# Kernel tuning notes

Measured on AMD Instinct MI355X. Metric: run time of the kernel, lower is better.

The kernel has to match this reference:

```python
import jax, jax.numpy as jnp
import numpy as np

NFEAT, NHID, NHEADS = 512, 64, 8
ALPHA = 0.2
NEG = -9e15  # torch uses -9000000000000000.0


def _xavier(key, shape, gain=1.414):
    fan_in, fan_out = shape[-2], shape[-1]
    bound = gain * np.sqrt(6.0 / (fan_in + fan_out))
    return jax.random.uniform(key, shape, jnp.float32, -bound, bound)


def setup_inputs() -> dict:
    key = jax.random.key(0)
    ks = jax.random.split(key, 6)
    N = 2048
    x = jax.random.normal(ks[0], (N, NFEAT), jnp.float32)
    adj = jax.random.randint(ks[1], (N, N), 0, 2, jnp.int32)
    # per-head stacked params for the two attention banks
    W1 = _xavier(ks[2], (NHEADS, NFEAT, NHID))
    a1 = _xavier(ks[3], (NHEADS, 2 * NHID, 1))
    W2 = _xavier(ks[4], (NHEADS, NFEAT, NHID))
    a2 = _xavier(ks[5], (NHEADS, 2 * NHID, 1))
    return {"x": x, "adj": adj, "W1": W1, "a1": a1, "W2": W2, "a2": a2}


def _gat_bank(x, adj_mask, W, a):
    """All heads of one GraphAttentionLayer bank, vectorized over heads.
    x: [N, F], W: [H, F, O], a: [H, 2O, 1]. Returns concat output [N, H*O]
    and attention [H, N, N]."""
    N = x.shape[0]
    Wh = jnp.einsum('nf,hfo->hno', x, W)               # [H, N, O]
    a_src = a[:, :NHID, 0]                             # [H, O]
    a_dst = a[:, NHID:, 0]                             # [H, O]
    Wh1 = jnp.einsum('hno,ho->hn', Wh, a_src)          # [H, N]
    Wh2 = jnp.einsum('hno,ho->hn', Wh, a_dst)          # [H, N]
    e = Wh1[:, :, None] + Wh2[:, None, :]              # [H, N, N]
    e = jnp.where(e > 0, e, ALPHA * e)                 # LeakyReLU
    e = jnp.where(adj_mask[None, :, :], e, NEG)
    attention = jax.nn.softmax(e, axis=-1)             # [H, N, N]
    h_prime = jnp.einsum('hnm,hmo->hno', attention, Wh)
    out = jax.nn.elu(h_prime)                          # concat=True -> elu
    # torch.cat over heads along feature dim: [N, H*O]
    out = jnp.transpose(out, (1, 0, 2)).reshape(N, NHEADS * NHID)
    return out, attention


def reference(x, adj, W1, a1, W2, a2):
    adj_mask = adj > 0
    # dropout layers are no-ops in eval mode
    h1, att1 = _gat_bank(x, adj_mask, W1, a1)
    h1 = jax.nn.elu(h1)
    h2, att2 = _gat_bank(h1, adj_mask, W2, a2)
    h2 = jax.nn.elu(h2)
    return h2, att1, att2
```

## Files before the change

kernel.cpp:

```cpp
#include <hip/hip_runtime.h>
#include <hip/hip_bf16.h>


typedef __attribute__((ext_vector_type(8))) short bf16x8;
typedef __attribute__((ext_vector_type(4))) float f32x4;

__device__ __forceinline__ float bf2f(unsigned short u) {
    return __uint_as_float(((unsigned int)u) << 16);
}
__device__ __forceinline__ unsigned short f2bf(float f) {
    __hip_bfloat16 h = __float2bfloat16(f);
    return __builtin_bit_cast(unsigned short, h);
}
__device__ __forceinline__ float elu1(float x) { return x > 0.f ? x : expm1f(x); }

__global__ __launch_bounds__(256) void adjbits_kernel(
    const int* __restrict__ adj, unsigned long long* __restrict__ gbits) {
    int g = blockIdx.x * 256 + threadIdx.x;
    unsigned long long m = __ballot(adj[g] > 0);
    if ((threadIdx.x & 63) == 0) gbits[g >> 6] = m;
}

__global__ __launch_bounds__(256) void reorder_w_kernel(
    const float* __restrict__ W, unsigned short* __restrict__ WpHi,
    unsigned short* __restrict__ WpLo) {
    int i = blockIdx.x * 256 + threadIdx.x;
    int o = i & 63;
    int k = (i >> 6) & 511;
    int h = i >> 15;
    float v = W[i];
    unsigned short hi = f2bf(v);
    unsigned short lo = f2bf(v - bf2f(hi));
    long idx = (((h * 16) + (k >> 5)) * 64 + o) * 32 + (k & 31);
    WpHi[idx] = hi;
    WpLo[idx] = lo;
}

__global__ __launch_bounds__(256, 2) void gemm1_kernel(
    const float* __restrict__ A,
    const unsigned short* __restrict__ BpHi, const unsigned short* __restrict__ BpLo,
    const float* __restrict__ avec,
    unsigned short* __restrict__ Whp, float* __restrict__ s1, float* __restrict__ s2) {
    __shared__ float accred[2][64][20];
    const int bx   = blockIdx.x;
    const int h    = bx >> 6;
    const int mt   = bx & 63;
    const int tid  = threadIdx.x;
    const int wave = tid >> 6;
    const int lane = tid & 63;
    const int quad = lane >> 4;
    const int m16  = lane & 15;
    const int rw   = wave & 1;
    const int kw   = wave >> 1;
    const int rowbase = mt * 32 + rw * 16;

    const float* Arow = A + (long)(rowbase + m16) * 512 + kw * 256 + quad * 8;
    const long boff = ((long)(h * 16 + kw * 8) * 64 + m16) * 32 + quad * 8;
    const unsigned short* BH = BpHi + boff;
    const unsigned short* BL = BpLo + boff;

    f32x4 acc[4];
#pragma unroll
    for (int t = 0; t < 4; ++t)
#pragma unroll
        for (int r = 0; r < 4; ++r) acc[t][r] = 0.f;

    for (int kb = 0; kb < 8; ++kb) {
        const float* ap = Arow + kb * 32;
        bf16x8 ahi, alo;
#pragma unroll
        for (int j = 0; j < 8; ++j) {
            float v = ap[j];
            unsigned short hv = f2bf(v);
            ahi[j] = (short)hv;
            alo[j] = (short)f2bf(v - bf2f(hv));
        }
        const unsigned short* bh0 = BH + (long)kb * 2048;
        const unsigned short* bl0 = BL + (long)kb * 2048;
#pragma unroll
        for (int t = 0; t < 4; ++t) {
            bf16x8 bh = *reinterpret_cast<const bf16x8*>(bh0 + t * 512);
            bf16x8 bl = *reinterpret_cast<const bf16x8*>(bl0 + t * 512);
            acc[t] = __builtin_amdgcn_mfma_f32_16x16x32_bf16(alo, bh, acc[t], 0, 0, 0);
            acc[t] = __builtin_amdgcn_mfma_f32_16x16x32_bf16(ahi, bl, acc[t], 0, 0, 0);
            acc[t] = __builtin_amdgcn_mfma_f32_16x16x32_bf16(ahi, bh, acc[t], 0, 0, 0);
        }
    }

    if (kw == 1) {
#pragma unroll
        for (int t = 0; t < 4; ++t)
            *reinterpret_cast<f32x4*>(&accred[rw][t * 16 + m16][quad * 4]) = acc[t];
    }
    __syncthreads();
    if (kw == 1) return;

#pragma unroll
    for (int t = 0; t < 4; ++t) {
        f32x4 o = *reinterpret_cast<const f32x4*>(&accred[rw][t * 16 + m16][quad * 4]);
#pragma unroll
        for (int r = 0; r < 4; ++r) acc[t][r] += o[r];
    }

    float aS[4], aD[4];
#pragma unroll
    for (int t = 0; t < 4; ++t) {
        aS[t] = avec[(h << 7) + t * 16 + m16];
        aD[t] = avec[(h << 7) + 64 + t * 16 + m16];
    }
#pragma unroll
    for (int r = 0; r < 4; ++r) {
        float t1 = 0.f, t2 = 0.f;
#pragma unroll
        for (int t = 0; t < 4; ++t) {
            float v = acc[t][r];
            t1 = fmaf(v, aS[t], t1);
            t2 = fmaf(v, aD[t], t2);
        }
#pragma unroll
        for (int off = 1; off < 16; off <<= 1) {
            t1 += __shfl_xor(t1, off);
            t2 += __shfl_xor(t2, off);
        }
        if (m16 == 0) {
            int row = rowbase + quad * 4 + r;
            s1[(h << 11) + row] = t1;
            s2[(h << 11) + row] = t2;
        }
    }

#pragma unroll
    for (int t = 0; t < 4; ++t) {
        const int col = t * 16 + m16;
#pragma unroll
        for (int r = 0; r < 4; ++r) {
            const int row = rowbase + quad * 4 + r;
            long idx = (((long)(h * 64 + (row >> 5)) * 64 + col) << 5) + (row & 31);
            Whp[idx] = f2bf(acc[t][r]);
        }
    }
}

__global__ __launch_bounds__(256, 4) void fused_att_kernel(
    const float* __restrict__ s1g, const float* __restrict__ s2g,
    const unsigned int* __restrict__ gbits,
    const unsigned short* __restrict__ Whp,
    float* __restrict__ att, float* __restrict__ hout) {
    __shared__ unsigned int lbits[16 * 65];
    __shared__ float ls2[2048];
    __shared__ float lmax[4][16];
    __shared__ float lsum[4][16];
    __shared__ float accred[3][64][20];
    __shared__ f32x4 pstage[4][16][9];

    const int bx   = blockIdx.x;
    const int h    = bx >> 7;
    const int row0 = (bx & 127) << 4;
    const int tid  = threadIdx.x;
    const int wq   = tid >> 6;
    const int lane = tid & 63;
    const int quad = lane >> 4;
    const int m16  = lane & 15;

#pragma unroll
    for (int i = 0; i < 4; ++i) {
        int idx = i * 256 + tid;
        lbits[(idx >> 6) * 65 + (idx & 63)] = gbits[((row0 + (idx >> 6)) << 6) + (idx & 63)];
    }
    const float4* s2v4 = reinterpret_cast<const float4*>(s2g + (h << 11));
#pragma unroll
    for (int i = 0; i < 2; ++i) {
        int idx = i * 256 + tid;
        reinterpret_cast<float4*>(ls2)[idx] = s2v4[idx];
    }
    __syncthreads();

    const float s1i = s1g[(h << 11) + row0 + m16];

    float mx = -INFINITY;
    for (int i = 0; i < 16; ++i) {
        const int jt = wq * 16 + i;
        unsigned int word = lbits[m16 * 65 + jt];
        float4 sa = *reinterpret_cast<const float4*>(ls2 + jt * 32 + quad * 8);
        float4 sb = *reinterpret_cast<const float4*>(ls2 + jt * 32 + quad * 8 + 4);
        float sv[8] = {sa.x, sa.y, sa.z, sa.w, sb.x, sb.y, sb.z, sb.w};
#pragma unroll
        for (int u = 0; u < 8; ++u)
            mx = fmaxf(mx, ((word >> (quad * 8 + u)) & 1u) ? sv[u] : -INFINITY);
    }
    mx = fmaxf(mx, __shfl_xor(mx, 16));
    mx = fmaxf(mx, __shfl_xor(mx, 32));
    if (lane < 16) lmax[wq][m16] = mx;
    __syncthreads();
    const float Ms2 = fmaxf(fmaxf(lmax[0][m16], lmax[1][m16]),
                            fmaxf(lmax[2][m16], lmax[3][m16]));
    const float ebar = s1i + Ms2;
    const float m = fmaxf(ebar, 0.2f * ebar);
    const bool am = (m == -INFINITY);

    float lp = 0.f;
    for (int i = 0; i < 16; ++i) {
        const int jt = wq * 16 + i;
        unsigned int word = lbits[m16 * 65 + jt];
        float4 sa = *reinterpret_cast<const float4*>(ls2 + jt * 32 + quad * 8);
        float4 sb = *reinterpret_cast<const float4*>(ls2 + jt * 32 + quad * 8 + 4);
        float sv[8] = {sa.x, sa.y, sa.z, sa.w, sb.x, sb.y, sb.z, sb.w};
#pragma unroll
        for (int u = 0; u < 8; ++u) {
            float e = s1i + sv[u];
            e = fmaxf(e, 0.2f * e);
            lp += ((word >> (quad * 8 + u)) & 1u) ? __expf(e - m) : 0.f;
        }
    }
    lp += __shfl_xor(lp, 16);
    lp += __shfl_xor(lp, 32);
    if (lane < 16) lsum[wq][m16] = lp;
    __syncthreads();
    const float l = lsum[0][m16] + lsum[1][m16] + lsum[2][m16] + lsum[3][m16];
    const float invl = am ? 0.f : 1.f / l;
    const float fallb = 1.f / 2048.f;

    f32x4 acc[4];
#pragma unroll
    for (int t = 0; t < 4; ++t)
#pragma unroll
        for (int r = 0; r < 4; ++r) acc[t][r] = 0.f;

    const unsigned short* BW = Whp + ((long)(h << 12) + m16) * 32 + quad * 8;
    float* attbase = att + (long)h * 4194304 + (long)row0 * 2048;
    const int fr = lane >> 3;
    const int fc = lane & 7;

    for (int i = 0; i < 16; ++i) {
        const int jt = wq * 16 + i;
        unsigned int word = lbits[m16 * 65 + jt];
        float4 sa = *reinterpret_cast<const float4*>(ls2 + jt * 32 + quad * 8);
        float4 sb = *reinterpret_cast<const float4*>(ls2 + jt * 32 + quad * 8 + 4);
        float sv[8] = {sa.x, sa.y, sa.z, sa.w, sb.x, sb.y, sb.z, sb.w};
        float p[8];
        bf16x8 af;
#pragma unroll
        for (int u = 0; u < 8; ++u) {
            float e = s1i + sv[u];
            e = fmaxf(e, 0.2f * e);
            float pv = ((word >> (quad * 8 + u)) & 1u) ? __expf(e - m) * invl : 0.f;
            p[u] = am ? fallb : pv;
            af[u] = (short)f2bf(p[u]);
        }
        f32x4 plo, phi;
        plo[0] = p[0]; plo[1] = p[1]; plo[2] = p[2]; plo[3] = p[3];
        phi[0] = p[4]; phi[1] = p[5]; phi[2] = p[6]; phi[3] = p[7];
        pstage[wq][m16][quad * 2]     = plo;
        pstage[wq][m16][quad * 2 + 1] = phi;

        const unsigned short* b0 = BW + (long)jt * 2048;
#pragma unroll
        for (int t = 0; t < 4; ++t) {
            bf16x8 bf = *reinterpret_cast<const bf16x8*>(b0 + t * 512);
            acc[t] = __builtin_amdgcn_mfma_f32_16x16x32_bf16(af, bf, acc[t], 0, 0, 0);
        }

#pragma unroll
        for (int half = 0; half < 2; ++half) {
            const int r = half * 8 + fr;
            f32x4 v = pstage[wq][r][fc];
            __builtin_nontemporal_store(
                v, reinterpret_cast<f32x4*>(attbase + (long)r * 2048 + jt * 32 + fc * 4));
        }
    }

    if (wq > 0) {
#pragma unroll
        for (int t = 0; t < 4; ++t)
            *reinterpret_cast<f32x4*>(&accred[wq - 1][t * 16 + m16][quad * 4]) = acc[t];
    }
    __syncthreads();
    if (wq == 0) {
#pragma unroll
        for (int t = 0; t < 4; ++t) {
            const int col = t * 16 + m16;
#pragma unroll
            for (int w = 0; w < 3; ++w) {
                f32x4 o = *reinterpret_cast<const f32x4*>(&accred[w][col][quad * 4]);
#pragma unroll
                for (int r = 0; r < 4; ++r) acc[t][r] += o[r];
            }
#pragma unroll
            for (int r = 0; r < 4; ++r) {
                const int row = row0 + quad * 4 + r;
                hout[(row << 9) + (h << 6) + col] = elu1(elu1(acc[t][r]));
            }
        }
    }
}

extern "C" void kernel_launch(void* const* d_in, const int* in_sizes, int n_in,
                              void* d_out, int out_size, void* d_ws, size_t ws_size,
                              hipStream_t stream) {
    const float* x  = (const float*)d_in[0];
    const int* adj  = (const int*)d_in[1];
    const float* W1 = (const float*)d_in[2];
    const float* a1 = (const float*)d_in[3];
    const float* W2 = (const float*)d_in[4];
    const float* a2 = (const float*)d_in[5];

    float* out  = (float*)d_out;
    float* att1 = out + 1048576;
    float* att2 = att1 + 33554432;

    char* w = (char*)d_ws;
    unsigned short* WpHi  = (unsigned short*)(w);
    unsigned short* WpLo  = (unsigned short*)(w + 524288);
    unsigned short* Whp   = (unsigned short*)(w + 1048576);
    float* s1             = (float*)(w + 3145728);
    float* s2             = (float*)(w + 3211264);
    unsigned long long* gbits = (unsigned long long*)(w + 3276800);
    float* x2             = (float*)(w + 3801088);

    const unsigned int* gbits32 = (const unsigned int*)gbits;

    adjbits_kernel<<<16384, 256, 0, stream>>>(adj, gbits);

    reorder_w_kernel<<<1024, 256, 0, stream>>>(W1, WpHi, WpLo);
    gemm1_kernel<<<512, 256, 0, stream>>>(x, WpHi, WpLo, a1, Whp, s1, s2);
    fused_att_kernel<<<1024, 256, 0, stream>>>(s1, s2, gbits32, Whp, att1, x2);

    reorder_w_kernel<<<1024, 256, 0, stream>>>(W2, WpHi, WpLo);
    gemm1_kernel<<<512, 256, 0, stream>>>(x2, WpHi, WpLo, a2, Whp, s1, s2);
    fused_att_kernel<<<1024, 256, 0, stream>>>(s1, s2, gbits32, Whp, att2, out);
}
```

Measured before the change: 358.6 us.

## Use global per-head s2 max as softmax shift and cache unnormalized exps

Computes a per-head global maximum of s2 in the GEMM epilogue via atomicMax on order-preserving keys, and uses it as the softmax shift. This removes the per-row masked max pass and one block barrier. The unnormalized exponentials are cached in registers as bf16 and fed directly to the MFMA, with normalization applied once to the output accumulators. This drops the second exp pass. The risks are more register pressure from the 16-entry cached array and possible underflow when the global max is far above a row's masked max. Written attention values are also now rounded through bf16 before scaling.

```diff
diff --git a/kernel.cpp b/kernel.cpp
--- a/kernel.cpp
+++ b/kernel.cpp
@@ -13,6 +13,14 @@
     return __builtin_bit_cast(unsigned short, h);
 }
 __device__ __forceinline__ float elu1(float x) { return x > 0.f ? x : expm1f(x); }
+
+__device__ __forceinline__ unsigned fkey(float f) {
+    unsigned b = __float_as_uint(f);
+    return (b & 0x80000000u) ? ~b : (b | 0x80000000u);
+}
+__device__ __forceinline__ float funkey(unsigned k) {
+    return __uint_as_float((k & 0x80000000u) ? (k ^ 0x80000000u) : ~k);
+}
 
 __global__ __launch_bounds__(256) void adjbits_kernel(
     const int* __restrict__ adj, unsigned long long* __restrict__ gbits) {
@@ -23,7 +31,8 @@
 
 __global__ __launch_bounds__(256) void reorder_w_kernel(
     const float* __restrict__ W, unsigned short* __restrict__ WpHi,
-    unsigned short* __restrict__ WpLo) {
+    unsigned short* __restrict__ WpLo, unsigned* __restrict__ Mmax) {
+    if (blockIdx.x == 0 && threadIdx.x < 8) Mmax[threadIdx.x] = 0u;
     int i = blockIdx.x * 256 + threadIdx.x;
     int o = i & 63;
     int k = (i >> 6) & 511;
@@ -40,7 +49,8 @@
     const float* __restrict__ A,
     const unsigned short* __restrict__ BpHi, const unsigned short* __restrict__ BpLo,
     const float* __restrict__ avec,
-    unsigned short* __restrict__ Whp, float* __restrict__ s1, float* __restrict__ s2) {
+    unsigned short* __restrict__ Whp, float* __restrict__ s1, float* __restrict__ s2,
+    unsigned* __restrict__ Mmax) {
     __shared__ float accred[2][64][20];
     const int bx   = blockIdx.x;
     const int h    = bx >> 6;
@@ -108,6 +118,7 @@
         aS[t] = avec[(h << 7) + t * 16 + m16];
         aD[t] = avec[(h << 7) + 64 + t * 16 + m16];
     }
+    float s2max = -INFINITY;
 #pragma unroll
     for (int r = 0; r < 4; ++r) {
         float t1 = 0.f, t2 = 0.f;
@@ -122,12 +133,16 @@
             t1 += __shfl_xor(t1, off);
             t2 += __shfl_xor(t2, off);
         }
+        s2max = fmaxf(s2max, t2);
         if (m16 == 0) {
             int row = rowbase + quad * 4 + r;
             s1[(h << 11) + row] = t1;
             s2[(h << 11) + row] = t2;
         }
     }
+    s2max = fmaxf(s2max, __shfl_xor(s2max, 16));
+    s2max = fmaxf(s2max, __shfl_xor(s2max, 32));
+    if (lane == 0) atomicMax(Mmax + h, fkey(s2max));
 
 #pragma unroll
     for (int t = 0; t < 4; ++t) {
@@ -145,11 +160,12 @@
     const float* __restrict__ s1g, const float* __restrict__ s2g,
     const unsigned int* __restrict__ gbits,
     const unsigned short* __restrict__ Whp,
+    const unsigned* __restrict__ Mmax,
     float* __restrict__ att, float* __restrict__ hout) {
     __shared__ unsigned int lbits[16 * 65];
     __shared__ float ls2[2048];
-    __shared__ float lmax[4][16];
     __shared__ float lsum[4][16];
+    __shared__ float linv[16];
     __shared__ float accred[3][64][20];
     __shared__ f32x4 pstage[4][16][9];
 
@@ -176,49 +192,39 @@
     __syncthreads();
 
     const float s1i = s1g[(h << 11) + row0 + m16];
-
-    float mx = -INFINITY;
+    const float M = funkey(Mmax[h]);
+    const float ebar = s1i + M;
+    const float m = fmaxf(ebar, 0.2f * ebar);
+
+    bf16x8 uarr[16];
+    float lp = 0.f;
+#pragma unroll
     for (int i = 0; i < 16; ++i) {
         const int jt = wq * 16 + i;
-        unsigned int word = lbits[m16 * 65 + jt];
+        unsigned int word = lbits[m16 * 65 + jt] >> (quad * 8);
         float4 sa = *reinterpret_cast<const float4*>(ls2 + jt * 32 + quad * 8);
         float4 sb = *reinterpret_cast<const float4*>(ls2 + jt * 32 + quad * 8 + 4);
         float sv[8] = {sa.x, sa.y, sa.z, sa.w, sb.x, sb.y, sb.z, sb.w};
-#pragma unroll
-        for (int u = 0; u < 8; ++u)
-            mx = fmaxf(mx, ((word >> (quad * 8 + u)) & 1u) ? sv[u] : -INFINITY);
-    }
-    mx = fmaxf(mx, __shfl_xor(mx, 16));
-    mx = fmaxf(mx, __shfl_xor(mx, 32));
-    if (lane < 16) lmax[wq][m16] = mx;
-    __syncthreads();
-    const float Ms2 = fmaxf(fmaxf(lmax[0][m16], lmax[1][m16]),
-                            fmaxf(lmax[2][m16], lmax[3][m16]));
-    const float ebar = s1i + Ms2;
-    const float m = fmaxf(ebar, 0.2f * ebar);
-    const bool am = (m == -INFINITY);
-
-    float lp = 0.f;
-    for (int i = 0; i < 16; ++i) {
-        const int jt = wq * 16 + i;
-        unsigned int word = lbits[m16 * 65 + jt];
-        float4 sa = *reinterpret_cast<const float4*>(ls2 + jt * 32 + quad * 8);
-        float4 sb = *reinterpret_cast<const float4*>(ls2 + jt * 32 + quad * 8 + 4);
-        float sv[8] = {sa.x, sa.y, sa.z, sa.w, sb.x, sb.y, sb.z, sb.w};
+        bf16x8 uf;
 #pragma unroll
         for (int u = 0; u < 8; ++u) {
             float e = s1i + sv[u];
             e = fmaxf(e, 0.2f * e);
-            lp += ((word >> (quad * 8 + u)) & 1u) ? __expf(e - m) : 0.f;
-        }
+            float ex = ((word >> u) & 1u) ? __expf(e - m) : 0.f;
+            lp += ex;
+            uf[u] = (short)f2bf(ex);
+        }
+        uarr[i] = uf;
     }
     lp += __shfl_xor(lp, 16);
     lp += __shfl_xor(lp, 32);
     if (lane < 16) lsum[wq][m16] = lp;
     __syncthreads();
     const float l = lsum[0][m16] + lsum[1][m16] + lsum[2][m16] + lsum[3][m16];
+    const bool am = (l == 0.f);
     const float invl = am ? 0.f : 1.f / l;
-    const float fallb = 1.f / 2048.f;
+    const float fb = am ? (1.f / 2048.f) : 0.f;
+    if (wq == 0 && lane < 16) linv[m16] = invl;
 
     f32x4 acc[4];
 #pragma unroll
@@ -231,22 +237,15 @@
     const int fr = lane >> 3;
     const int fc = lane & 7;
 
+#pragma unroll
     for (int i = 0; i < 16; ++i) {
         const int jt = wq * 16 + i;
-        unsigned int word = lbits[m16 * 65 + jt];
-        float4 sa = *reinterpret_cast<const float4*>(ls2 + jt * 32 + quad * 8);
-        float4 sb = *reinterpret_cast<const float4*>(ls2 + jt * 32 + quad * 8 + 4);
-        float sv[8] = {sa.x, sa.y, sa.z, sa.w, sb.x, sb.y, sb.z, sb.w};
+        bf16x8 uf = uarr[i];
         float p[8];
-        bf16x8 af;
-#pragma unroll
-        for (int u = 0; u < 8; ++u) {
-            float e = s1i + sv[u];
-            e = fmaxf(e, 0.2f * e);
-            float pv = ((word >> (quad * 8 + u)) & 1u) ? __expf(e - m) * invl : 0.f;
-            p[u] = am ? fallb : pv;
-            af[u] = (short)f2bf(p[u]);
-        }
+#pragma unroll
+        for (int u = 0; u < 8; ++u)
+            p[u] = fmaf(bf2f((unsigned short)uf[u]), invl, fb);
+
         f32x4 plo, phi;
         plo[0] = p[0]; plo[1] = p[1]; plo[2] = p[2]; plo[3] = p[3];
         phi[0] = p[4]; phi[1] = p[5]; phi[2] = p[6]; phi[3] = p[7];
@@ -257,7 +256,7 @@
 #pragma unroll
         for (int t = 0; t < 4; ++t) {
             bf16x8 bf = *reinterpret_cast<const bf16x8*>(b0 + t * 512);
-            acc[t] = __builtin_amdgcn_mfma_f32_16x16x32_bf16(af, bf, acc[t], 0, 0, 0);
+            acc[t] = __builtin_amdgcn_mfma_f32_16x16x32_bf16(uf, bf, acc[t], 0, 0, 0);
         }
 
 #pragma unroll
@@ -288,7 +287,8 @@
 #pragma unroll
             for (int r = 0; r < 4; ++r) {
                 const int row = row0 + quad * 4 + r;
-                hout[(row << 9) + (h << 6) + col] = elu1(elu1(acc[t][r]));
+                const float sc = linv[quad * 4 + r];
+                hout[(row << 9) + (h << 6) + col] = elu1(elu1(acc[t][r] * sc));
             }
         }
     }
@@ -316,16 +316,17 @@
     float* s2             = (float*)(w + 3211264);
     unsigned long long* gbits = (unsigned long long*)(w + 3276800);
     float* x2             = (float*)(w + 3801088);
+    unsigned* Mmax        = (unsigned*)(w + 7995392);
 
     const unsigned int* gbits32 = (const unsigned int*)gbits;
 
     adjbits_kernel<<<16384, 256, 0, stream>>>(adj, gbits);
 
-    reorder_w_kernel<<<1024, 256, 0, stream>>>(W1, WpHi, WpLo);
-    gemm1_kernel<<<512, 256, 0, stream>>>(x, WpHi, WpLo, a1, Whp, s1, s2);
-    fused_att_kernel<<<1024, 256, 0, stream>>>(s1, s2, gbits32, Whp, att1, x2);
-
-    reorder_w_kernel<<<1024, 256, 0, stream>>>(W2, WpHi, WpLo);
-    gemm1_kernel<<<512, 256, 0, stream>>>(x2, WpHi, WpLo, a2, Whp, s1, s2);
-    fused_att_kernel<<<1024, 256, 0, stream>>>(s1, s2, gbits32, Whp, att2, out);
-}
+    reorder_w_kernel<<<1024, 256, 0, stream>>>(W1, WpHi, WpLo, Mmax);
+    gemm1_kernel<<<512, 256, 0, stream>>>(x, WpHi, WpLo, a1, Whp, s1, s2, Mmax);
+    fused_att_kernel<<<1024, 256, 0, stream>>>(s1, s2, gbits32, Whp, Mmax, att1, x2);
+
+    reorder_w_kernel<<<1024, 256, 0, stream>>>(W2, WpHi, WpLo, Mmax);
+    gemm1_kernel<<<512, 256, 0, stream>>>(x2, WpHi, WpLo, a2, Whp, s1, s2, Mmax);
+    fused_att_kernel<<<1024, 256, 0, stream>>>(s1, s2, gbits32, Whp, Mmax, att2, out);
+}
```

Measured after the change: 405.7 us. 1.13x slower.
